# Kernel optimization log

Hardware: AMD Instinct MI355X
Metric: run time of the kernel (lower is better)

Reference implementation:

```python
import jax, jax.numpy as jnp
import numpy as np

T = 32        # time_step
H = 64        # n_hidden (and dense width)
A = 8         # nb_actions
OBS_DIM = 512
B = 4096      # sequences; obs rows = B*T
LN_EPS = 1e-12  # tf.contrib.layers.layer_norm epsilon


def setup_inputs() -> dict:
    key = jax.random.key(0)
    ks = jax.random.split(key, 10)
    s = 0.1
    return {
        "obs":  jax.random.normal(ks[0], (B * T, OBS_DIM), jnp.float32),
        "W0":   jax.random.normal(ks[1], (OBS_DIM, H), jnp.float32) * s,
        "b0":   jnp.zeros((H,), jnp.float32),
        "gamma": jnp.ones((H,), jnp.float32),
        "beta":  jnp.zeros((H,), jnp.float32),
        "Wfw":  jax.random.normal(ks[2], (2 * H, 4 * H), jnp.float32) * s,
        "bfw":  jnp.zeros((4 * H,), jnp.float32),
        "Wbw":  jax.random.normal(ks[3], (2 * H, 4 * H), jnp.float32) * s,
        "bbw":  jnp.zeros((4 * H,), jnp.float32),
        "Wc":   jax.random.uniform(ks[4], (H, A), jnp.float32, -0.003, 0.003),
        "bc":   jnp.zeros((A,), jnp.float32),
    }


def _lstm_scan(xs, W, b):
    """BasicLSTMCell (forget_bias=1.0). xs: [T, B, H] -> hs: [T, B, H]."""
    nb = xs.shape[1]
    init = (jnp.zeros((nb, H), xs.dtype), jnp.zeros((nb, H), xs.dtype))

    def step(carry, x_t):
        c, h = carry
        z = jnp.concatenate([x_t, h], axis=-1) @ W + b  # [B, 4H]
        i, j, f, o = jnp.split(z, 4, axis=-1)           # TF gate order i,j,f,o
        c = c * jax.nn.sigmoid(f + 1.0) + jax.nn.sigmoid(i) * jnp.tanh(j)
        h = jnp.tanh(c) * jax.nn.sigmoid(o)
        return (c, h), h

    _, hs = jax.lax.scan(step, init, xs)
    return hs


def reference(obs, W0, b0, gamma, beta, Wfw, bfw, Wbw, bbw, Wc, bc):
    # dense(64) + layer_norm + relu
    x = obs @ W0 + b0                                   # [B*T, H]
    mu = jnp.mean(x, axis=-1, keepdims=True)
    var = jnp.mean(jnp.square(x - mu), axis=-1, keepdims=True)
    x = gamma * (x - mu) / jnp.sqrt(var + LN_EPS) + beta
    x = jax.nn.relu(x)

    xt = x.reshape(-1, T, H).transpose(1, 0, 2)          # [T, B, H]
    hs_fw = _lstm_scan(xt, Wfw, bfw)                     # [T, B, H]
    hs_bw = _lstm_scan(xt[::-1], Wbw, bbw)[::-1]         # reverse-in, reverse-out

    # tf.reshape on the (fw, bw) tuple stacks along a new leading axis:
    # [2, B, T, H] -> [2B, T*H, 1]; conv1d(kernel=stride=H) == per-step proj.
    y = jnp.stack([hs_fw.transpose(1, 0, 2), hs_bw.transpose(1, 0, 2)], axis=0)
    y = y.reshape(-1, T, H)                              # [2B, T, H]
    out = jnp.tanh(jnp.einsum('btk,ka->bta', y, Wc) + bc)  # [2B, T, A]
    return out
```

## Files before the change

kernel.cpp:

```cpp
#include <hip/hip_runtime.h>
#include <hip/hip_bf16.h>

typedef __attribute__((ext_vector_type(8))) short bf16x8;
typedef __attribute__((ext_vector_type(4))) float f32x4;

#define MFMA_BF16 __builtin_amdgcn_mfma_f32_16x16x32_bf16

#define GLDS16(gp, lp)                                                        \
  __builtin_amdgcn_global_load_lds(                                           \
      (const __attribute__((address_space(1))) void*)(gp),                    \
      (__attribute__((address_space(3))) void*)(lp), 16, 0, 0)

__device__ __forceinline__ unsigned pk2(float a, float b) {
  __hip_bfloat162 t = __float22bfloat162_rn(make_float2(a, b));
  return *reinterpret_cast<unsigned*>(&t);
}
__device__ __forceinline__ unsigned short f2bf_hw(float f) {
  __hip_bfloat16 h = __float2bfloat16(f);
  return *reinterpret_cast<unsigned short*>(&h);
}
__device__ __forceinline__ float tanh_f(float x) {
  return 1.f - 2.f * __builtin_amdgcn_rcpf(1.f + __expf(2.f * x));
}

__global__ void k0_conv(const float* __restrict__ W0, const float* __restrict__ Wfw,
                        const float* __restrict__ Wbw, unsigned short* __restrict__ wfrag,
                        unsigned short* __restrict__ wlstm) {
  int gid = blockIdx.x * 256 + threadIdx.x;
  if (gid < 4096) {
    int f = gid >> 6, l = gid & 63;
    int k0 = (f >> 2) * 32 + ((l >> 4) << 3);
    int n = (f & 3) * 16 + (l & 15);
    bf16x8 v;
#pragma unroll
    for (int j = 0; j < 8; ++j) v[j] = (short)f2bf_hw(W0[(k0 + j) * 64 + n]);
    *(bf16x8*)(wfrag + gid * 8) = v;
  } else if (gid < 12288) {
    int g2 = gid - 4096;
    const float* W = (g2 < 4096) ? Wfw : Wbw;
    int f = (g2 & 4095) >> 6, l = g2 & 63;
    int wv = f >> 4, gate = (f >> 2) & 3, kf = f & 3;
    int col = gate * 64 + wv * 16 + (l & 15);
    int kr = kf * 32 + ((l >> 4) << 3);
    bf16x8 v;
#pragma unroll
    for (int j = 0; j < 8; ++j) v[j] = (short)f2bf_hw(W[(kr + j) * 256 + col]);
    *(bf16x8*)(wlstm + g2 * 8) = v;
  }
}

__global__ __launch_bounds__(256, 3) void k_dense_ln(
    const float* __restrict__ obs, const unsigned short* __restrict__ wfrag,
    const float* __restrict__ b0, const float* __restrict__ gam,
    const float* __restrict__ bet, unsigned short* __restrict__ xout) {
  __shared__ __align__(16) char lds[49152];
  const int tid = threadIdx.x, w = tid >> 6, l = tid & 63;
  const int g = l >> 4, c = l & 15;
  const int tile = (blockIdx.x & 7) * 256 + (blockIdx.x >> 3);
  const long blk64 = (long)tile * 64;
  const long rb = blk64 + w * 16;

  float b0v[4], gv[4], bv[4];
#pragma unroll
  for (int nt = 0; nt < 4; ++nt) {
    int col = nt * 16 + c;
    b0v[nt] = b0[col]; gv[nt] = gam[col]; bv[nt] = bet[col];
  }
  const unsigned short* wfl = wfrag + l * 8;
  const char* gB = (const char*)obs + blk64 * 2048;

  const int rlo = w * 4 + g;
  asm volatile("s_waitcnt vmcnt(0)" ::: "memory");

#define K1_STAGE(q)                                                           \
  {                                                                           \
    _Pragma("unroll") for (int i = 0; i < 4; ++i) {                           \
      int row_ = i * 16 + rlo;                                                \
      const char* gp_ = gB + (long)row_ * 2048 + (q) * 256 +                  \
                        (long)((c ^ rlo) * 16);                               \
      char* lp_ = lds + ((q) % 3) * 16384 + (i * 4096 + (w * 64 + l) * 16);   \
      GLDS16(gp_, lp_);                                                       \
    }                                                                         \
  }

  K1_STAGE(0);
  K1_STAGE(1);
  K1_STAGE(2);

  f32x4 acc[4];
#pragma unroll
  for (int nt = 0; nt < 4; ++nt) acc[nt] = (f32x4){0.f, 0.f, 0.f, 0.f};

#pragma unroll
  for (int q = 0; q < 8; ++q) {
    constexpr int VW[8] = {8, 16, 24, 24, 24, 24, 20, 16};
    asm volatile("s_waitcnt vmcnt(%0)" :: "i"(VW[q]) : "memory");
    __builtin_amdgcn_s_barrier();
    __builtin_amdgcn_sched_barrier(0);

    const char* rowb = lds + (q % 3) * 16384 + (w * 16 + c) * 256;
#pragma unroll
    for (int kf = 0; kf < 2; ++kf) {
      int fb = (q * 2 + kf) * 4;
      bf16x8 B0 = *(const bf16x8*)(wfl + (fb + 0) * 512);
      bf16x8 B1 = *(const bf16x8*)(wfl + (fb + 1) * 512);
      bf16x8 B2 = *(const bf16x8*)(wfl + (fb + 2) * 512);
      bf16x8 B3 = *(const bf16x8*)(wfl + (fb + 3) * 512);
      int u0 = kf * 8 + g * 2;
      float4 f0 = *(const float4*)(rowb + ((u0 + 0) ^ c) * 16);
      float4 f1 = *(const float4*)(rowb + ((u0 + 1) ^ c) * 16);
      union { bf16x8 v; unsigned u[4]; } af;
      af.u[0] = pk2(f0.x, f0.y); af.u[1] = pk2(f0.z, f0.w);
      af.u[2] = pk2(f1.x, f1.y); af.u[3] = pk2(f1.z, f1.w);
      acc[0] = MFMA_BF16(af.v, B0, acc[0], 0, 0, 0);
      acc[1] = MFMA_BF16(af.v, B1, acc[1], 0, 0, 0);
      acc[2] = MFMA_BF16(af.v, B2, acc[2], 0, 0, 0);
      acc[3] = MFMA_BF16(af.v, B3, acc[3], 0, 0, 0);
    }
    if (q < 5) {
      __builtin_amdgcn_s_barrier();
      __builtin_amdgcn_sched_barrier(0);
      K1_STAGE(q + 3);
    }
  }

  float vv[4][4], s1[4], s2[4];
#pragma unroll
  for (int r = 0; r < 4; ++r) { s1[r] = 0.f; s2[r] = 0.f; }
#pragma unroll
  for (int nt = 0; nt < 4; ++nt)
#pragma unroll
    for (int r = 0; r < 4; ++r) {
      float val = acc[nt][r] + b0v[nt];
      vv[nt][r] = val; s1[r] += val; s2[r] += val * val;
    }
#pragma unroll
  for (int r = 0; r < 4; ++r) {
#pragma unroll
    for (int m = 1; m <= 8; m <<= 1) {
      s1[r] += __shfl_xor(s1[r], m);
      s2[r] += __shfl_xor(s2[r], m);
    }
  }
  unsigned short* xw = (unsigned short*)lds + w * 1024;
#pragma unroll
  for (int r = 0; r < 4; ++r) {
    float mu = s1[r] * 0.015625f;
    float var = s2[r] * 0.015625f - mu * mu;
    float inv = rsqrtf(var + 1e-12f);
    int row = g * 4 + r;
#pragma unroll
    for (int nt = 0; nt < 4; ++nt) {
      float xn = (vv[nt][r] - mu) * inv * gv[nt] + bv[nt];
      xw[(row * 64 + nt * 16 + c) ^ (g << 3)] = f2bf_hw(fmaxf(xn, 0.f));
    }
  }
#pragma unroll
  for (int m2 = 0; m2 < 2; ++m2) {
    int m = m2 * 64 + l;
    int row = m >> 3, u8 = m & 7;
    bf16x8 v = *(const bf16x8*)(xw + ((row * 64 + u8 * 8) ^ ((row >> 2) << 3)));
    *(bf16x8*)(xout + (rb + row) * 64 + u8 * 8) = v;
  }
}

__global__ __launch_bounds__(256, 2) void k_lstm(
    const unsigned short* __restrict__ x, const unsigned short* __restrict__ wlstm,
    const float* __restrict__ bfw, const float* __restrict__ bbw,
    const float* __restrict__ Wc, const float* __restrict__ bc,
    float* __restrict__ out) {
  __shared__ __align__(16) char xl[65536];
  __shared__ unsigned short hl[2 * 1024];
  const int tid = threadIdx.x, w = tid >> 6, l = tid & 63;
  const int g = l >> 4, c = l & 15;
  const int bid = blockIdx.x;
  const int kk = bid >> 3;
  const int dir = kk & 1;
  const int g2 = (bid & 7) * 32 + (kk >> 1);
  const int sq = g2 * 16;
  const float* bias = dir ? bbw : bfw;

  bf16x8 Bf[4][4];
  const unsigned short* wl = wlstm + ((long)dir * 4096 + w * 16 * 64) * 8;
#pragma unroll
  for (int gate = 0; gate < 4; ++gate)
#pragma unroll
    for (int kf = 0; kf < 4; ++kf)
      Bf[gate][kf] = *(const bf16x8*)(wl + ((gate * 4 + kf) * 64 + l) * 8);
  float bz[4];
#pragma unroll
  for (int gate = 0; gate < 4; ++gate) bz[gate] = bias[gate * 64 + w * 16 + c];

  bf16x8 Pc[2];
#pragma unroll
  for (int kf = 0; kf < 2; ++kf)
#pragma unroll
    for (int j = 0; j < 8; ++j) Pc[kf][j] = 0;
  float bcv = 0.f;
  if (c < 8) {
#pragma unroll
    for (int kf = 0; kf < 2; ++kf)
#pragma unroll
      for (int j = 0; j < 8; ++j)
        Pc[kf][j] = (short)f2bf_hw(Wc[(kf * 32 + g * 8 + j) * 8 + c]);
    bcv = bc[c];
  }

  asm volatile("s_waitcnt vmcnt(0)" ::: "memory");

  const int ss = l >> 3, sc = l & 7;
#pragma unroll
  for (int j = 0; j < 8; ++j) {
    int tt = w * 8 + j;
    int te = dir ? 31 - tt : tt;
#pragma unroll
    for (int p = 0; p < 2; ++p) {
      int s = p * 8 + ss;
      const char* gp = (const char*)x +
          ((long)(sq + s) * 32 + te) * 128 + (long)(sc ^ (s & 7)) * 16;
      char* lp = xl + tt * 2048 + p * 1024;
      GLDS16(gp, lp);
    }
  }

  for (int i = tid; i < 1024; i += 256) ((unsigned*)hl)[i] = 0u;
  float cs[4] = {0.f, 0.f, 0.f, 0.f};

  if (w == 0) asm volatile("s_waitcnt vmcnt(12)" ::: "memory");
  asm volatile("s_waitcnt lgkmcnt(0)" ::: "memory");
  __builtin_amdgcn_s_barrier();
  __builtin_amdgcn_sched_barrier(0);

  const int hq = w >> 1;
  const int hgp = ((w & 1) * 2 + (c >> 3)) * 16;
  const int hlo = c & 7;

  f32x4 accx[4];
  {
    const char* xt = xl + 0 * 2048 + c * 128;
    bf16x8 Ax0 = *(const bf16x8*)(xt + (long)((g) ^ (c & 7)) * 16);
    bf16x8 Ax1 = *(const bf16x8*)(xt + (long)((4 + g) ^ (c & 7)) * 16);
#pragma unroll
    for (int gate = 0; gate < 4; ++gate) {
      f32x4 b = (f32x4){bz[gate], bz[gate], bz[gate], bz[gate]};
      accx[gate] = MFMA_BF16(Ax1, Bf[gate][1],
                             MFMA_BF16(Ax0, Bf[gate][0], b, 0, 0, 0), 0, 0, 0);
    }
  }
  asm volatile("s_waitcnt lgkmcnt(0)" ::: "memory");
  __builtin_amdgcn_s_barrier();
  __builtin_amdgcn_sched_barrier(0);

  int p = 0;
#pragma unroll
  for (int t = 0; t < 32; ++t) {
    bf16x8 Ah0 = *(const bf16x8*)((const char*)hl + p * 2048 + l * 16);
    bf16x8 Ah1 = *(const bf16x8*)((const char*)hl + p * 2048 + 1024 + l * 16);

    f32x4 acc[4];
#pragma unroll
    for (int gate = 0; gate < 4; ++gate)
      acc[gate] = MFMA_BF16(Ah1, Bf[gate][3],
                            MFMA_BF16(Ah0, Bf[gate][2], accx[gate], 0, 0, 0),
                            0, 0, 0);

    if (t + 1 < 32) {
      const char* xt = xl + (t + 1) * 2048 + c * 128;
      bf16x8 Ax0 = *(const bf16x8*)(xt + (long)((g) ^ (c & 7)) * 16);
      bf16x8 Ax1 = *(const bf16x8*)(xt + (long)((4 + g) ^ (c & 7)) * 16);
#pragma unroll
      for (int gate = 0; gate < 4; ++gate) {
        f32x4 b = (f32x4){bz[gate], bz[gate], bz[gate], bz[gate]};
        accx[gate] = MFMA_BF16(Ax1, Bf[gate][1],
                               MFMA_BF16(Ax0, Bf[gate][0], b, 0, 0, 0), 0, 0, 0);
      }
    }

    const int wb = (p ^ 1) * 1024;
    unsigned short* xh = (unsigned short*)xl + t * 1024;
#pragma unroll
    for (int r = 0; r < 4; ++r) {
      float ei = __expf(-acc[0][r]);
      float ej = __expf(2.f * acc[1][r]);
      float ef = __expf(-(acc[2][r] + 1.f));
      float eo = __expf(-acc[3][r]);
      float p12 = (1.f + ei) * (1.f + ej);
      float r3 = __builtin_amdgcn_rcpf(p12 * (1.f + ef));
      float it = (ej - 1.f) * (1.f + ef) * r3;
      float sf = p12 * r3;
      cs[r] = cs[r] * sf + it;
      float ec = __expf(2.f * cs[r]);
      float r2 = __builtin_amdgcn_rcpf((1.f + eo) * (1.f + ec));
      unsigned short hb = f2bf_hw((ec - 1.f) * r2);
      int off = (hq * 64 + hgp + 4 * g + r) * 8 + hlo;
      hl[wb + off] = hb;
      xh[off] = hb;
    }

    if (t + 2 < 32) {
      if (w == ((t + 2) >> 3))
        asm volatile("s_waitcnt vmcnt(%0)" :: "i"(14 - 2 * ((t + 2) & 7)) : "memory");
    }
    asm volatile("s_waitcnt lgkmcnt(0)" ::: "memory");
    __builtin_amdgcn_s_barrier();
    __builtin_amdgcn_sched_barrier(0);
    p ^= 1;
  }

#pragma unroll
  for (int j = 0; j < 8; ++j) {
    int t = w * 8 + j;
    const char* hb = xl + t * 2048;
    bf16x8 Ph0 = *(const bf16x8*)(hb + l * 16);
    bf16x8 Ph1 = *(const bf16x8*)(hb + 1024 + l * 16);
    f32x4 pa = (f32x4){0.f, 0.f, 0.f, 0.f};
    pa = MFMA_BF16(Ph0, Pc[0], pa, 0, 0, 0);
    pa = MFMA_BF16(Ph1, Pc[1], pa, 0, 0, 0);
    if (c < 8) {
      int tp = dir ? 31 - t : t;
#pragma unroll
      for (int r = 0; r < 4; ++r) {
        long orow = (long)dir * 4096 + sq + 4 * g + r;
        out[(orow * 32 + tp) * 8 + c] = tanh_f(pa[r] + bcv);
      }
    }
  }
}

extern "C" void kernel_launch(void* const* d_in, const int* in_sizes, int n_in,
                              void* d_out, int out_size, void* d_ws, size_t ws_size,
                              hipStream_t stream) {
  const float* obs = (const float*)d_in[0];
  const float* W0  = (const float*)d_in[1];
  const float* b0  = (const float*)d_in[2];
  const float* gam = (const float*)d_in[3];
  const float* bet = (const float*)d_in[4];
  const float* Wfw = (const float*)d_in[5];
  const float* bfw = (const float*)d_in[6];
  const float* Wbw = (const float*)d_in[7];
  const float* bbw = (const float*)d_in[8];
  const float* Wc  = (const float*)d_in[9];
  const float* bc  = (const float*)d_in[10];
  float* out = (float*)d_out;

  unsigned short* wfrag = (unsigned short*)d_ws;
  unsigned short* wlstm = wfrag + 4096 * 8;
  unsigned short* xbf   = wlstm + 8192 * 8;

  k0_conv<<<48, 256, 0, stream>>>(W0, Wfw, Wbw, wfrag, wlstm);
  k_dense_ln<<<2048, 256, 0, stream>>>(obs, wfrag, b0, gam, bet, xbf);
  k_lstm<<<512, 256, 0, stream>>>(xbf, wlstm, bfw, bbw, Wc, bc, out);
}
```

Measured before the change: 97.53 us.

## Fuse forward and backward LSTM directions into one block with staged output

Each block now runs both LSTM directions for its 16 sequences, so the shared x tile is loaded once for both and the grid is halved to 256 blocks with one block per CU. Wave 0 computes the output projection for the previous step inside the recurrence loop, writing into a shared staging buffer that is then flushed to global memory with coalesced float4 stores. This drops the duplicate x loads and the post-loop projection pass, and gives each step's serial chain two independent directions of work to interleave. In exchange, register pressure roughly doubles, occupancy falls, there are only 256 blocks (roughly one per CU), and x is no longer streamed in per timestep before the loop starts.

```diff
diff --git a/kernel.cpp b/kernel.cpp
--- a/kernel.cpp
+++ b/kernel.cpp
@@ -164,32 +164,33 @@
   }
 }
 
-__global__ __launch_bounds__(256, 2) void k_lstm(
+__global__ __launch_bounds__(256, 1) void k_lstm(
     const unsigned short* __restrict__ x, const unsigned short* __restrict__ wlstm,
     const float* __restrict__ bfw, const float* __restrict__ bbw,
     const float* __restrict__ Wc, const float* __restrict__ bc,
     float* __restrict__ out) {
   __shared__ __align__(16) char xl[65536];
-  __shared__ unsigned short hl[2 * 1024];
+  __shared__ unsigned short hl[2][2048];
+  __shared__ float pl[2][16 * 32 * 8];
   const int tid = threadIdx.x, w = tid >> 6, l = tid & 63;
   const int g = l >> 4, c = l & 15;
   const int bid = blockIdx.x;
-  const int kk = bid >> 3;
-  const int dir = kk & 1;
-  const int g2 = (bid & 7) * 32 + (kk >> 1);
+  const int g2 = (bid & 7) * 32 + (bid >> 3);
   const int sq = g2 * 16;
-  const float* bias = dir ? bbw : bfw;
-
-  bf16x8 Bf[4][4];
-  const unsigned short* wl = wlstm + ((long)dir * 4096 + w * 16 * 64) * 8;
-#pragma unroll
-  for (int gate = 0; gate < 4; ++gate)
-#pragma unroll
-    for (int kf = 0; kf < 4; ++kf)
-      Bf[gate][kf] = *(const bf16x8*)(wl + ((gate * 4 + kf) * 64 + l) * 8);
-  float bz[4];
-#pragma unroll
-  for (int gate = 0; gate < 4; ++gate) bz[gate] = bias[gate * 64 + w * 16 + c];
+
+  bf16x8 Bf[2][4][4];
+  float bz[2][4];
+#pragma unroll
+  for (int d = 0; d < 2; ++d) {
+    const unsigned short* wl = wlstm + ((long)d * 4096 + w * 16 * 64) * 8;
+#pragma unroll
+    for (int gate = 0; gate < 4; ++gate) {
+#pragma unroll
+      for (int kf = 0; kf < 4; ++kf)
+        Bf[d][gate][kf] = *(const bf16x8*)(wl + ((gate * 4 + kf) * 64 + l) * 8);
+      bz[d][gate] = (d ? bbw : bfw)[gate * 64 + w * 16 + c];
+    }
+  }
 
   bf16x8 Pc[2];
 #pragma unroll
@@ -212,21 +213,20 @@
 #pragma unroll
   for (int j = 0; j < 8; ++j) {
     int tt = w * 8 + j;
-    int te = dir ? 31 - tt : tt;
 #pragma unroll
     for (int p = 0; p < 2; ++p) {
       int s = p * 8 + ss;
       const char* gp = (const char*)x +
-          ((long)(sq + s) * 32 + te) * 128 + (long)(sc ^ (s & 7)) * 16;
+          ((long)(sq + s) * 32 + tt) * 128 + (long)(sc ^ (s & 7)) * 16;
       char* lp = xl + tt * 2048 + p * 1024;
       GLDS16(gp, lp);
     }
   }
 
-  for (int i = tid; i < 1024; i += 256) ((unsigned*)hl)[i] = 0u;
-  float cs[4] = {0.f, 0.f, 0.f, 0.f};
-
-  if (w == 0) asm volatile("s_waitcnt vmcnt(12)" ::: "memory");
+  for (int i = tid; i < 2048; i += 256) ((unsigned*)hl)[i] = 0u;
+  float cs[2][4] = {{0.f, 0.f, 0.f, 0.f}, {0.f, 0.f, 0.f, 0.f}};
+
+  asm volatile("s_waitcnt vmcnt(0)" ::: "memory");
   asm volatile("s_waitcnt lgkmcnt(0)" ::: "memory");
   __builtin_amdgcn_s_barrier();
   __builtin_amdgcn_sched_barrier(0);
@@ -234,96 +234,128 @@
   const int hq = w >> 1;
   const int hgp = ((w & 1) * 2 + (c >> 3)) * 16;
   const int hlo = c & 7;
-
-  f32x4 accx[4];
-  {
-    const char* xt = xl + 0 * 2048 + c * 128;
+  const int hoff = (hq * 64 + hgp) * 8 + hlo;
+
+  f32x4 accx[2][4];
+#pragma unroll
+  for (int d = 0; d < 2; ++d) {
+    const char* xt = xl + (d ? 31 : 0) * 2048 + c * 128;
     bf16x8 Ax0 = *(const bf16x8*)(xt + (long)((g) ^ (c & 7)) * 16);
     bf16x8 Ax1 = *(const bf16x8*)(xt + (long)((4 + g) ^ (c & 7)) * 16);
 #pragma unroll
     for (int gate = 0; gate < 4; ++gate) {
-      f32x4 b = (f32x4){bz[gate], bz[gate], bz[gate], bz[gate]};
-      accx[gate] = MFMA_BF16(Ax1, Bf[gate][1],
-                             MFMA_BF16(Ax0, Bf[gate][0], b, 0, 0, 0), 0, 0, 0);
-    }
-  }
-  asm volatile("s_waitcnt lgkmcnt(0)" ::: "memory");
-  __builtin_amdgcn_s_barrier();
-  __builtin_amdgcn_sched_barrier(0);
+      f32x4 b = (f32x4){bz[d][gate], bz[d][gate], bz[d][gate], bz[d][gate]};
+      accx[d][gate] = MFMA_BF16(Ax1, Bf[d][gate][1],
+                                MFMA_BF16(Ax0, Bf[d][gate][0], b, 0, 0, 0),
+                                0, 0, 0);
+    }
+  }
 
   int p = 0;
-#pragma unroll
+#pragma unroll 2
   for (int t = 0; t < 32; ++t) {
-    bf16x8 Ah0 = *(const bf16x8*)((const char*)hl + p * 2048 + l * 16);
-    bf16x8 Ah1 = *(const bf16x8*)((const char*)hl + p * 2048 + 1024 + l * 16);
-
-    f32x4 acc[4];
-#pragma unroll
-    for (int gate = 0; gate < 4; ++gate)
-      acc[gate] = MFMA_BF16(Ah1, Bf[gate][3],
-                            MFMA_BF16(Ah0, Bf[gate][2], accx[gate], 0, 0, 0),
-                            0, 0, 0);
+    bf16x8 Ah[2][2];
+#pragma unroll
+    for (int d = 0; d < 2; ++d) {
+      const char* hb = (const char*)&hl[d][0] + p * 2048;
+      Ah[d][0] = *(const bf16x8*)(hb + l * 16);
+      Ah[d][1] = *(const bf16x8*)(hb + 1024 + l * 16);
+    }
+
+    if (t >= 1 && w == 0) {
+#pragma unroll
+      for (int d = 0; d < 2; ++d) {
+        f32x4 pa = (f32x4){0.f, 0.f, 0.f, 0.f};
+        pa = MFMA_BF16(Ah[d][0], Pc[0], pa, 0, 0, 0);
+        pa = MFMA_BF16(Ah[d][1], Pc[1], pa, 0, 0, 0);
+        if (c < 8) {
+          int tp = d ? 32 - t : t - 1;
+#pragma unroll
+          for (int r = 0; r < 4; ++r)
+            pl[d][(4 * g + r) * 256 + tp * 8 + c] = tanh_f(pa[r] + bcv);
+        }
+      }
+    }
+
+    f32x4 acc[2][4];
+#pragma unroll
+    for (int d = 0; d < 2; ++d)
+#pragma unroll
+      for (int gate = 0; gate < 4; ++gate)
+        acc[d][gate] = MFMA_BF16(Ah[d][1], Bf[d][gate][3],
+                                 MFMA_BF16(Ah[d][0], Bf[d][gate][2],
+                                           accx[d][gate], 0, 0, 0),
+                                 0, 0, 0);
 
     if (t + 1 < 32) {
-      const char* xt = xl + (t + 1) * 2048 + c * 128;
-      bf16x8 Ax0 = *(const bf16x8*)(xt + (long)((g) ^ (c & 7)) * 16);
-      bf16x8 Ax1 = *(const bf16x8*)(xt + (long)((4 + g) ^ (c & 7)) * 16);
-#pragma unroll
-      for (int gate = 0; gate < 4; ++gate) {
-        f32x4 b = (f32x4){bz[gate], bz[gate], bz[gate], bz[gate]};
-        accx[gate] = MFMA_BF16(Ax1, Bf[gate][1],
-                               MFMA_BF16(Ax0, Bf[gate][0], b, 0, 0, 0), 0, 0, 0);
+#pragma unroll
+      for (int d = 0; d < 2; ++d) {
+        const char* xt = xl + (d ? 30 - t : t + 1) * 2048 + c * 128;
+        bf16x8 Ax0 = *(const bf16x8*)(xt + (long)((g) ^ (c & 7)) * 16);
+        bf16x8 Ax1 = *(const bf16x8*)(xt + (long)((4 + g) ^ (c & 7)) * 16);
+#pragma unroll
+        for (int gate = 0; gate < 4; ++gate) {
+          f32x4 b = (f32x4){bz[d][gate], bz[d][gate], bz[d][gate], bz[d][gate]};
+          accx[d][gate] = MFMA_BF16(Ax1, Bf[d][gate][1],
+                                    MFMA_BF16(Ax0, Bf[d][gate][0], b, 0, 0, 0),
+                                    0, 0, 0);
+        }
       }
     }
 
     const int wb = (p ^ 1) * 1024;
-    unsigned short* xh = (unsigned short*)xl + t * 1024;
-#pragma unroll
-    for (int r = 0; r < 4; ++r) {
-      float ei = __expf(-acc[0][r]);
-      float ej = __expf(2.f * acc[1][r]);
-      float ef = __expf(-(acc[2][r] + 1.f));
-      float eo = __expf(-acc[3][r]);
-      float p12 = (1.f + ei) * (1.f + ej);
-      float r3 = __builtin_amdgcn_rcpf(p12 * (1.f + ef));
-      float it = (ej - 1.f) * (1.f + ef) * r3;
-      float sf = p12 * r3;
-      cs[r] = cs[r] * sf + it;
-      float ec = __expf(2.f * cs[r]);
-      float r2 = __builtin_amdgcn_rcpf((1.f + eo) * (1.f + ec));
-      unsigned short hb = f2bf_hw((ec - 1.f) * r2);
-      int off = (hq * 64 + hgp + 4 * g + r) * 8 + hlo;
-      hl[wb + off] = hb;
-      xh[off] = hb;
-    }
-
-    if (t + 2 < 32) {
-      if (w == ((t + 2) >> 3))
-        asm volatile("s_waitcnt vmcnt(%0)" :: "i"(14 - 2 * ((t + 2) & 7)) : "memory");
-    }
+#pragma unroll
+    for (int d = 0; d < 2; ++d)
+#pragma unroll
+      for (int r = 0; r < 4; ++r) {
+        float ei = __expf(-acc[d][0][r]);
+        float ej = __expf(2.f * acc[d][1][r]);
+        float ef = __expf(-(acc[d][2][r] + 1.f));
+        float eo = __expf(-acc[d][3][r]);
+        float p12 = (1.f + ei) * (1.f + ej);
+        float r3 = __builtin_amdgcn_rcpf(p12 * (1.f + ef));
+        float it = (ej - 1.f) * (1.f + ef) * r3;
+        float sf = p12 * r3;
+        cs[d][r] = cs[d][r] * sf + it;
+        float ec = __expf(2.f * cs[d][r]);
+        float r2 = __builtin_amdgcn_rcpf((1.f + eo) * (1.f + ec));
+        hl[d][wb + hoff + (4 * g + r) * 8] = f2bf_hw((ec - 1.f) * r2);
+      }
+
     asm volatile("s_waitcnt lgkmcnt(0)" ::: "memory");
     __builtin_amdgcn_s_barrier();
     __builtin_amdgcn_sched_barrier(0);
     p ^= 1;
   }
 
-#pragma unroll
-  for (int j = 0; j < 8; ++j) {
-    int t = w * 8 + j;
-    const char* hb = xl + t * 2048;
-    bf16x8 Ph0 = *(const bf16x8*)(hb + l * 16);
-    bf16x8 Ph1 = *(const bf16x8*)(hb + 1024 + l * 16);
-    f32x4 pa = (f32x4){0.f, 0.f, 0.f, 0.f};
-    pa = MFMA_BF16(Ph0, Pc[0], pa, 0, 0, 0);
-    pa = MFMA_BF16(Ph1, Pc[1], pa, 0, 0, 0);
-    if (c < 8) {
-      int tp = dir ? 31 - t : t;
-#pragma unroll
-      for (int r = 0; r < 4; ++r) {
-        long orow = (long)dir * 4096 + sq + 4 * g + r;
-        out[(orow * 32 + tp) * 8 + c] = tanh_f(pa[r] + bcv);
+  if (w == 0) {
+#pragma unroll
+    for (int d = 0; d < 2; ++d) {
+      const char* hb = (const char*)&hl[d][0] + p * 2048;
+      bf16x8 Ph0 = *(const bf16x8*)(hb + l * 16);
+      bf16x8 Ph1 = *(const bf16x8*)(hb + 1024 + l * 16);
+      f32x4 pa = (f32x4){0.f, 0.f, 0.f, 0.f};
+      pa = MFMA_BF16(Ph0, Pc[0], pa, 0, 0, 0);
+      pa = MFMA_BF16(Ph1, Pc[1], pa, 0, 0, 0);
+      if (c < 8) {
+        int tp = d ? 0 : 31;
+#pragma unroll
+        for (int r = 0; r < 4; ++r)
+          pl[d][(4 * g + r) * 256 + tp * 8 + c] = tanh_f(pa[r] + bcv);
       }
     }
+  }
+
+  asm volatile("s_waitcnt lgkmcnt(0)" ::: "memory");
+  __builtin_amdgcn_s_barrier();
+#pragma unroll
+  for (int i = 0; i < 8; ++i) {
+    int fi = tid + i * 256;
+    int d = fi >> 10, rem = fi & 1023;
+    int s = rem >> 6, r2 = rem & 63;
+    int t2 = r2 >> 1, a4 = (r2 & 1) * 4;
+    float4 v = *(const float4*)(&pl[d][0] + s * 256 + t2 * 8 + a4);
+    *(float4*)(out + ((long)(d * 4096 + sq + s) * 32 + t2) * 8 + a4) = v;
   }
 }
 
@@ -349,5 +381,5 @@
 
   k0_conv<<<48, 256, 0, stream>>>(W0, Wfw, Wbw, wfrag, wlstm);
   k_dense_ln<<<2048, 256, 0, stream>>>(obs, wfrag, b0, gam, bet, xbf);
-  k_lstm<<<512, 256, 0, stream>>>(xbf, wlstm, bfw, bbw, Wc, bc, out);
-}
+  k_lstm<<<256, 256, 0, stream>>>(xbf, wlstm, bfw, bbw, Wc, bc, out);
+}
```

After: 109.4 us. +12.2%, slower.

## Restructure dense+LN kernel: register-resident weights, column-split waves, row-stage pipeline

Applied to the files above, without the earlier changes.

The dense+layernorm kernel now keeps each wave's whole 16-column slice of the bf16 W0 fragments in registers and splits work across waves by output column instead of by row. The obs tile is streamed in four 16-row stages of the full 512-wide K, double-buffered in a 64 KB LDS region. Because each wave now owns only part of every row, layernorm statistics are reduced across waves through a small shared buffer, which adds an extra barrier per stage. The intent is to stop re-reading weight fragments from global memory on every K step, at the cost of more registers, larger LDS, and occupancy lowered from 3 to 2 blocks per CU.

```diff
diff --git a/kernel.cpp b/kernel.cpp
--- a/kernel.cpp
+++ b/kernel.cpp
@@ -49,118 +49,107 @@
   }
 }
 
-__global__ __launch_bounds__(256, 3) void k_dense_ln(
+__global__ __launch_bounds__(256, 2) void k_dense_ln(
     const float* __restrict__ obs, const unsigned short* __restrict__ wfrag,
     const float* __restrict__ b0, const float* __restrict__ gam,
     const float* __restrict__ bet, unsigned short* __restrict__ xout) {
-  __shared__ __align__(16) char lds[49152];
+  __shared__ __align__(16) char lds[65536];
+  __shared__ __align__(16) float red[16][2][4];
+  __shared__ __align__(16) unsigned short xb[4][16][16];
   const int tid = threadIdx.x, w = tid >> 6, l = tid & 63;
   const int g = l >> 4, c = l & 15;
   const int tile = (blockIdx.x & 7) * 256 + (blockIdx.x >> 3);
-  const long blk64 = (long)tile * 64;
-  const long rb = blk64 + w * 16;
-
-  float b0v[4], gv[4], bv[4];
-#pragma unroll
-  for (int nt = 0; nt < 4; ++nt) {
-    int col = nt * 16 + c;
-    b0v[nt] = b0[col]; gv[nt] = gam[col]; bv[nt] = bet[col];
-  }
-  const unsigned short* wfl = wfrag + l * 8;
-  const char* gB = (const char*)obs + blk64 * 2048;
-
-  const int rlo = w * 4 + g;
+  const long R0 = (long)tile * 64;
+
+  bf16x8 Bf[16];
+#pragma unroll
+  for (int kf = 0; kf < 16; ++kf)
+    Bf[kf] = *(const bf16x8*)(wfrag + ((kf * 4 + w) * 64 + l) * 8);
+  const int col = w * 16 + c;
+  const float b0v = b0[col], gvv = gam[col], bvv = bet[col];
+
   asm volatile("s_waitcnt vmcnt(0)" ::: "memory");
-
-#define K1_STAGE(q)                                                           \
+  __builtin_amdgcn_sched_barrier(0);
+
+  const char* gB = (const char*)obs + R0 * 2048;
+#define K1_STAGE(st)                                                          \
   {                                                                           \
-    _Pragma("unroll") for (int i = 0; i < 4; ++i) {                           \
-      int row_ = i * 16 + rlo;                                                \
-      const char* gp_ = gB + (long)row_ * 2048 + (q) * 256 +                  \
-                        (long)((c ^ rlo) * 16);                               \
-      char* lp_ = lds + ((q) % 3) * 16384 + (i * 4096 + (w * 64 + l) * 16);   \
+    _Pragma("unroll") for (int i = 0; i < 8; ++i) {                           \
+      int q_ = w * 8 + i;                                                     \
+      int r_ = q_ >> 1, h_ = q_ & 1;                                          \
+      const char* gp_ = gB + (st) * 32768 + (long)r_ * 2048 +                 \
+                        (long)((h_ * 64 + (l ^ (r_ & 7))) * 16);              \
+      char* lp_ = lds + ((st) & 1) * 32768 + q_ * 1024;                       \
       GLDS16(gp_, lp_);                                                       \
     }                                                                         \
   }
 
   K1_STAGE(0);
   K1_STAGE(1);
-  K1_STAGE(2);
-
-  f32x4 acc[4];
-#pragma unroll
-  for (int nt = 0; nt < 4; ++nt) acc[nt] = (f32x4){0.f, 0.f, 0.f, 0.f};
-
-#pragma unroll
-  for (int q = 0; q < 8; ++q) {
-    constexpr int VW[8] = {8, 16, 24, 24, 24, 24, 20, 16};
-    asm volatile("s_waitcnt vmcnt(%0)" :: "i"(VW[q]) : "memory");
+
+#pragma unroll
+  for (int st = 0; st < 4; ++st) {
+    constexpr int VW[4] = {8, 9, 9, 1};
+    asm volatile("s_waitcnt vmcnt(%0)" :: "i"(VW[st]) : "memory");
     __builtin_amdgcn_s_barrier();
     __builtin_amdgcn_sched_barrier(0);
 
-    const char* rowb = lds + (q % 3) * 16384 + (w * 16 + c) * 256;
-#pragma unroll
-    for (int kf = 0; kf < 2; ++kf) {
-      int fb = (q * 2 + kf) * 4;
-      bf16x8 B0 = *(const bf16x8*)(wfl + (fb + 0) * 512);
-      bf16x8 B1 = *(const bf16x8*)(wfl + (fb + 1) * 512);
-      bf16x8 B2 = *(const bf16x8*)(wfl + (fb + 2) * 512);
-      bf16x8 B3 = *(const bf16x8*)(wfl + (fb + 3) * 512);
+    const char* rowb = lds + (st & 1) * 32768 + c * 2048;
+    f32x4 acc = (f32x4){0.f, 0.f, 0.f, 0.f};
+#pragma unroll
+    for (int kf = 0; kf < 16; ++kf) {
       int u0 = kf * 8 + g * 2;
-      float4 f0 = *(const float4*)(rowb + ((u0 + 0) ^ c) * 16);
-      float4 f1 = *(const float4*)(rowb + ((u0 + 1) ^ c) * 16);
+      float4 f0 = *(const float4*)(rowb + (long)(((u0 + 0) ^ (c & 7)) * 16));
+      float4 f1 = *(const float4*)(rowb + (long)(((u0 + 1) ^ (c & 7)) * 16));
       union { bf16x8 v; unsigned u[4]; } af;
       af.u[0] = pk2(f0.x, f0.y); af.u[1] = pk2(f0.z, f0.w);
       af.u[2] = pk2(f1.x, f1.y); af.u[3] = pk2(f1.z, f1.w);
-      acc[0] = MFMA_BF16(af.v, B0, acc[0], 0, 0, 0);
-      acc[1] = MFMA_BF16(af.v, B1, acc[1], 0, 0, 0);
-      acc[2] = MFMA_BF16(af.v, B2, acc[2], 0, 0, 0);
-      acc[3] = MFMA_BF16(af.v, B3, acc[3], 0, 0, 0);
-    }
-    if (q < 5) {
-      __builtin_amdgcn_s_barrier();
-      __builtin_amdgcn_sched_barrier(0);
-      K1_STAGE(q + 3);
-    }
-  }
-
-  float vv[4][4], s1[4], s2[4];
-#pragma unroll
-  for (int r = 0; r < 4; ++r) { s1[r] = 0.f; s2[r] = 0.f; }
-#pragma unroll
-  for (int nt = 0; nt < 4; ++nt)
+      acc = MFMA_BF16(af.v, Bf[kf], acc, 0, 0, 0);
+    }
+
+    float vv[4], s1[4], s2[4];
 #pragma unroll
     for (int r = 0; r < 4; ++r) {
-      float val = acc[nt][r] + b0v[nt];
-      vv[nt][r] = val; s1[r] += val; s2[r] += val * val;
-    }
-#pragma unroll
-  for (int r = 0; r < 4; ++r) {
-#pragma unroll
-    for (int m = 1; m <= 8; m <<= 1) {
-      s1[r] += __shfl_xor(s1[r], m);
-      s2[r] += __shfl_xor(s2[r], m);
-    }
-  }
-  unsigned short* xw = (unsigned short*)lds + w * 1024;
-#pragma unroll
-  for (int r = 0; r < 4; ++r) {
-    float mu = s1[r] * 0.015625f;
-    float var = s2[r] * 0.015625f - mu * mu;
-    float inv = rsqrtf(var + 1e-12f);
-    int row = g * 4 + r;
-#pragma unroll
-    for (int nt = 0; nt < 4; ++nt) {
-      float xn = (vv[nt][r] - mu) * inv * gv[nt] + bv[nt];
-      xw[(row * 64 + nt * 16 + c) ^ (g << 3)] = f2bf_hw(fmaxf(xn, 0.f));
-    }
-  }
-#pragma unroll
-  for (int m2 = 0; m2 < 2; ++m2) {
-    int m = m2 * 64 + l;
-    int row = m >> 3, u8 = m & 7;
-    bf16x8 v = *(const bf16x8*)(xw + ((row * 64 + u8 * 8) ^ ((row >> 2) << 3)));
-    *(bf16x8*)(xout + (rb + row) * 64 + u8 * 8) = v;
+      vv[r] = acc[r] + b0v;
+      s1[r] = vv[r]; s2[r] = vv[r] * vv[r];
+    }
+#pragma unroll
+    for (int r = 0; r < 4; ++r) {
+#pragma unroll
+      for (int m = 1; m <= 8; m <<= 1) {
+        s1[r] += __shfl_xor(s1[r], m);
+        s2[r] += __shfl_xor(s2[r], m);
+      }
+    }
+    if (c == 0) {
+#pragma unroll
+      for (int r = 0; r < 4; ++r) {
+        red[4 * g + r][0][w] = s1[r];
+        red[4 * g + r][1][w] = s2[r];
+      }
+    }
+    asm volatile("s_waitcnt lgkmcnt(0)" ::: "memory");
+    __builtin_amdgcn_s_barrier();
+    __builtin_amdgcn_sched_barrier(0);
+
+#pragma unroll
+    for (int r = 0; r < 4; ++r) {
+      float4 a = *(const float4*)&red[4 * g + r][0][0];
+      float4 b = *(const float4*)&red[4 * g + r][1][0];
+      float S1 = (a.x + a.y) + (a.z + a.w);
+      float S2 = (b.x + b.y) + (b.z + b.w);
+      float mu = S1 * 0.015625f;
+      float var = S2 * 0.015625f - mu * mu;
+      float inv = rsqrtf(var + 1e-12f);
+      float xn = (vv[r] - mu) * inv * gvv + bvv;
+      xb[w][4 * g + r][c] = f2bf_hw(fmaxf(xn, 0.f));
+    }
+    if (l < 32) {
+      int row = l >> 1, half = l & 1;
+      bf16x8 v = *(const bf16x8*)&xb[w][row][half * 8];
+      *(bf16x8*)(xout + (R0 + st * 16 + row) * 64 + w * 16 + half * 8) = v;
+    }
+    if (st + 2 < 4) K1_STAGE(st + 2);
   }
 }
 
```

Measured after the change: 104.7 us. 7.4% more time.
